# Kernel tuning notes

Hardware: AMD Instinct MI355X
Metric: run time of the kernel (lower is better)

## Reference

```python
import jax, jax.numpy as jnp
import numpy as np
from jax import lax

T, B, D = 200, 1024, 128  # max_len, batch, units (= input feature dim)


def setup_inputs() -> dict:
    key = jax.random.key(0)
    ks = jax.random.split(key, 16)
    s = 1.0 / np.sqrt(D)
    inp = {
        "inputs": jax.random.normal(ks[0], (T, B, D), dtype=jnp.float32),
        "state": jnp.zeros((B, D), dtype=jnp.float32),
        "att_score": jax.random.uniform(ks[1], (T, B, 1), dtype=jnp.float32),
        # binary validity mask [B, T], float because it multiplies the state
        "mask": (jax.random.uniform(ks[2], (B, T)) < 0.9).astype(jnp.float32),
        "max_len": T,
        # u gate (Bilinear: Dense(a) with bias + Dense(b) no bias)
        "Wau": jax.random.normal(ks[3], (D, D), dtype=jnp.float32) * s,
        "bau": jnp.zeros((D,), dtype=jnp.float32),
        "Wbu": jax.random.normal(ks[4], (D, D), dtype=jnp.float32) * s,
        # r gate
        "War": jax.random.normal(ks[5], (D, D), dtype=jnp.float32) * s,
        "bar": jnp.zeros((D,), dtype=jnp.float32),
        "Wbr": jax.random.normal(ks[6], (D, D), dtype=jnp.float32) * s,
        # candidate memory
        "Wac": jax.random.normal(ks[7], (D, D), dtype=jnp.float32) * s,
        "bac": jnp.zeros((D,), dtype=jnp.float32),
        "Wbc": jax.random.normal(ks[8], (D, D), dtype=jnp.float32) * s,
    }
    return inp


def reference(inputs, state, att_score, mask, max_len,
              Wau, bau, Wbu, War, bar, Wbr, Wac, bac, Wbc):
    # time-major mask [T, B, 1]
    mask_t = jnp.swapaxes(mask, 0, 1)[:, :, None]

    def step(s, xs):
        x, a, m = xs  # x:[B,D], a:[B,1], m:[B,1]
        u = jax.nn.sigmoid(x @ Wau + bau + s @ Wbu)
        r = jax.nn.sigmoid(x @ War + bar + s @ Wbr)
        c = jnp.tanh(x @ Wac + bac + r * (s @ Wbc))
        u_ = a * u
        new = (1.0 - u_) * s + u_ * c
        s = new * m + s * (1.0 - m)
        return s, None

    final_state, _ = lax.scan(step, state, (inputs, att_score, mask_t))
    return final_state
```

## Files before the change

### kernel.cpp

```cpp
#include <hip/hip_runtime.h>
#include <stdint.h>

#define T_LEN 200
#define B_SZ  1024
#define D_DIM 128
#define LOG2E 1.44269504088896340736f

typedef __bf16 bf16_t;
typedef __bf16 bf16x8 __attribute__((ext_vector_type(8)));
typedef float  f32x4  __attribute__((ext_vector_type(4)));

union BF8 { bf16x8 v; bf16_t e[8]; };

__device__ inline float rcp_f(float x) { return __builtin_amdgcn_rcpf(x); }

__device__ inline uint32_t cvt_pk_bf16(float a, float b) {
  uint32_t r;
  asm("v_cvt_pk_bf16_f32 %0, %1, %2" : "=v"(r) : "v"(a), "v"(b));
  return r;
}

#define BAR_LDS() asm volatile("s_waitcnt lgkmcnt(0)\n\ts_barrier" ::: "memory")

__global__ __launch_bounds__(512, 2) void augru_fused(
    const float* __restrict__ x,
    const float* __restrict__ state,
    const float* __restrict__ att,
    const float* __restrict__ mask,
    const float* __restrict__ Wau, const float* __restrict__ bau,
    const float* __restrict__ Wbu,
    const float* __restrict__ War, const float* __restrict__ bar,
    const float* __restrict__ Wbr,
    const float* __restrict__ Wac, const float* __restrict__ bac,
    const float* __restrict__ Wbc,
    float* __restrict__ out)
{
  __shared__ bf16_t xb[2][2048];
  __shared__ bf16_t sb[2][2048];
  __shared__ float  am_lds[(T_LEN + 1) * 16];

  const int tid = threadIdx.x;
  const int w  = tid >> 6;
  const int l  = tid & 63;
  const int lm = l & 15;
  const int lg = l >> 4;
  const int bb = blockIdx.x;
  const int R0 = bb * 16;
  const int col = w * 16 + lm;

  BF8 xu[4], xr[4], xc[4];
  BF8 su[4], sr[4], sc[4];
#pragma unroll
  for (int kk = 0; kk < 4; ++kk) {
#pragma unroll
    for (int j = 0; j < 8; ++j) {
      int k = kk * 32 + lg * 8 + j;
      xu[kk].e[j] = (bf16_t)(Wau[k * 128 + col] * LOG2E);
      xr[kk].e[j] = (bf16_t)(War[k * 128 + col] * LOG2E);
      xc[kk].e[j] = (bf16_t)(Wac[k * 128 + col] * (2.0f * LOG2E));
      su[kk].e[j] = (bf16_t)(Wbu[k * 128 + col] * LOG2E);
      sr[kk].e[j] = (bf16_t)(Wbr[k * 128 + col] * LOG2E);
      sc[kk].e[j] = (bf16_t)(Wbc[k * 128 + col] * (2.0f * LOG2E));
    }
  }
  const float b_u = bau[col] * LOG2E;
  const float b_r = bar[col] * LOG2E;
  const float b_c = bac[col] * (2.0f * LOG2E);

  const f32x4 biasU = {b_u, b_u, b_u, b_u};
  const f32x4 biasR = {b_r, b_r, b_r, b_r};
  const f32x4 biasC = {b_c, b_c, b_c, b_c};
  const f32x4 zero4 = {0.f, 0.f, 0.f, 0.f};

  for (int idx = tid; idx < (T_LEN + 1) * 16; idx += 512) {
    int t = idx >> 4; if (t > T_LEN - 1) t = T_LEN - 1;
    int row = idx & 15;
    am_lds[idx] = rcp_f(att[t * B_SZ + R0 + row] * mask[(R0 + row) * T_LEN + t]);
  }

  float sreg[4];
#pragma unroll
  for (int i = 0; i < 4; ++i)
    sreg[i] = state[(R0 + lg * 4 + i) * 128 + col];

  for (int idx = tid; idx < 2048; idx += 512) {
    int row = idx >> 7, k = idx & 127;
    sb[0][(k >> 3) * 128 + (row ^ (2 * ((k >> 3) & 1))) * 8 + (k & 7)] =
        (bf16_t)state[(R0 + row) * 128 + k];
  }

  const int srow = tid & 15;
  const int sc4  = tid >> 4;
  const int stg_pos = (sc4 >> 1) * 128 + srow * 8 + (sc4 & 1) * 4;
  const float* xrow = x + (size_t)(R0 + srow) * 128 + sc4 * 4;
  const size_t xstep = (size_t)B_SZ * 128;
  const size_t xoff_max = (size_t)(T_LEN - 1) * xstep;

  {
    float4 v0 = *(const float4*)(xrow);
    float4 v1 = *(const float4*)(xrow + xstep);
    uint2 p0, p1;
    p0.x = cvt_pk_bf16(v0.x, v0.y); p0.y = cvt_pk_bf16(v0.z, v0.w);
    p1.x = cvt_pk_bf16(v1.x, v1.y); p1.y = cvt_pk_bf16(v1.z, v1.w);
    *(uint2*)&xb[0][stg_pos] = p0;
    *(uint2*)&xb[1][stg_pos] = p1;
  }
  float4 xqA = *(const float4*)(xrow + 2 * xstep);
  float4 xqB = *(const float4*)(xrow + 3 * xstep);
  size_t offA = 4 * xstep;
  size_t offB = 5 * xstep;

  __syncthreads();

  f32x4 gU, gR, gC;
  {
    bf16x8 ax[4];
#pragma unroll
    for (int kk = 0; kk < 4; ++kk)
      ax[kk] = *(const bf16x8*)&xb[0][kk * 512 + 8 * l];
    gU = __builtin_amdgcn_mfma_f32_16x16x32_bf16(ax[0], xu[0].v, biasU, 0, 0, 0);
    gR = __builtin_amdgcn_mfma_f32_16x16x32_bf16(ax[0], xr[0].v, biasR, 0, 0, 0);
    gC = __builtin_amdgcn_mfma_f32_16x16x32_bf16(ax[0], xc[0].v, biasC, 0, 0, 0);
#pragma unroll
    for (int kk = 1; kk < 4; ++kk) {
      gU = __builtin_amdgcn_mfma_f32_16x16x32_bf16(ax[kk], xu[kk].v, gU, 0, 0, 0);
      gR = __builtin_amdgcn_mfma_f32_16x16x32_bf16(ax[kk], xr[kk].v, gR, 0, 0, 0);
      gC = __builtin_amdgcn_mfma_f32_16x16x32_bf16(ax[kk], xc[kk].v, gC, 0, 0, 0);
    }
  }
  union F4 { float4 v; float e[4]; } amv, amn;
  amv.v = *(const float4*)&am_lds[lg * 4];
  const float* am_ptr = &am_lds[16 + lg * 4];

  const int lx8   = 8 * (l ^ (2 * (lg & 1)));
  const int psi   = 2 * ((col >> 3) & 1);
  const int wbase = (col >> 3) * 128 + lg * 32 + (col & 7);

  BAR_LDS();

  auto step = [&](int t, float4& xq, size_t& xoff) {
    const int rp = t & 1;

    bf16x8 as_[4];
#pragma unroll
    for (int kk = 0; kk < 4; ++kk)
      as_[kk] = *(const bf16x8*)&sb[rp][kk * 512 + lx8];

    f32x4 aR = __builtin_amdgcn_mfma_f32_16x16x32_bf16(as_[0], sr[0].v, gR, 0, 0, 0);
    f32x4 bC = __builtin_amdgcn_mfma_f32_16x16x32_bf16(as_[0], sc[0].v, zero4, 0, 0, 0);
    f32x4 aU = __builtin_amdgcn_mfma_f32_16x16x32_bf16(as_[0], su[0].v, gU, 0, 0, 0);
#pragma unroll
    for (int kk = 1; kk < 4; ++kk) {
      aR = __builtin_amdgcn_mfma_f32_16x16x32_bf16(as_[kk], sr[kk].v, aR, 0, 0, 0);
      bC = __builtin_amdgcn_mfma_f32_16x16x32_bf16(as_[kk], sc[kk].v, bC, 0, 0, 0);
      aU = __builtin_amdgcn_mfma_f32_16x16x32_bf16(as_[kk], su[kk].v, aU, 0, 0, 0);
    }

    bf16_t* wbuf = sb[rp ^ 1];
#pragma unroll
    for (int i = 0; i < 4; ++i) {
      float Xr = __builtin_amdgcn_exp2f(-aR[i]);
      float Xu = __builtin_amdgcn_exp2f(-aU[i]);
      float r  = rcp_f(1.0f + Xr);
      float k  = rcp_f(fmaf(Xu, amv.e[i], amv.e[i]));
      float wc = fmaf(r, bC[i], gC[i]);
      float cg = fmaf(-2.0f, rcp_f(__builtin_amdgcn_exp2f(wc) + 1.0f), 1.0f);
      float sf = fmaf(k, cg - sreg[i], sreg[i]);
      sreg[i] = sf;
      wbuf[wbase + 8 * (i ^ psi)] = (bf16_t)sf;
    }

    bf16x8 ax[4];
#pragma unroll
    for (int kk = 0; kk < 4; ++kk)
      ax[kk] = *(const bf16x8*)&xb[rp ^ 1][kk * 512 + 8 * l];

    f32x4 nU = __builtin_amdgcn_mfma_f32_16x16x32_bf16(ax[0], xu[0].v, biasU, 0, 0, 0);
    f32x4 nR = __builtin_amdgcn_mfma_f32_16x16x32_bf16(ax[0], xr[0].v, biasR, 0, 0, 0);
    f32x4 nC = __builtin_amdgcn_mfma_f32_16x16x32_bf16(ax[0], xc[0].v, biasC, 0, 0, 0);
#pragma unroll
    for (int kk = 1; kk < 4; ++kk) {
      nU = __builtin_amdgcn_mfma_f32_16x16x32_bf16(ax[kk], xu[kk].v, nU, 0, 0, 0);
      nR = __builtin_amdgcn_mfma_f32_16x16x32_bf16(ax[kk], xr[kk].v, nR, 0, 0, 0);
      nC = __builtin_amdgcn_mfma_f32_16x16x32_bf16(ax[kk], xc[kk].v, nC, 0, 0, 0);
    }

    {
      uint2 p;
      p.x = cvt_pk_bf16(xq.x, xq.y);
      p.y = cvt_pk_bf16(xq.z, xq.w);
      *(uint2*)&xb[rp][stg_pos] = p;
    }
    xq = *(const float4*)(xrow + xoff);
    xoff += 2 * xstep; if (xoff > xoff_max) xoff = xoff_max;

    amn.v = *(const float4*)am_ptr;
    am_ptr += 16;

    gU = nU; gR = nR; gC = nC;
    amv.v = amn.v;

    BAR_LDS();
  };

#pragma unroll 1
  for (int t = 0; t < T_LEN; t += 2) {
    step(t,     xqA, offA);
    step(t + 1, xqB, offB);
  }

#pragma unroll
  for (int i = 0; i < 4; ++i)
    out[(R0 + lg * 4 + i) * 128 + col] = sreg[i];
}

extern "C" void kernel_launch(void* const* d_in, const int* in_sizes, int n_in,
                              void* d_out, int out_size, void* d_ws, size_t ws_size,
                              hipStream_t stream)
{
  const float* x    = (const float*)d_in[0];
  const float* st   = (const float*)d_in[1];
  const float* att  = (const float*)d_in[2];
  const float* mask = (const float*)d_in[3];
  const float* Wau  = (const float*)d_in[5];
  const float* bau  = (const float*)d_in[6];
  const float* Wbu  = (const float*)d_in[7];
  const float* War  = (const float*)d_in[8];
  const float* bar  = (const float*)d_in[9];
  const float* Wbr  = (const float*)d_in[10];
  const float* Wac  = (const float*)d_in[11];
  const float* bac  = (const float*)d_in[12];
  const float* Wbc  = (const float*)d_in[13];

  (void)d_ws; (void)ws_size;

  augru_fused<<<dim3(64), dim3(512), 0, stream>>>(
      x, st, att, mask, Wau, bau, Wbu, War, bar, Wbr, Wac, bac, Wbc,
      (float*)d_out);
}
```

Baseline: 294.1 us.

## Load x fragments directly into MFMA registers, dropping LDS staging of inputs

The input sequence x is now read from global memory straight into each lane's MFMA operand layout (8 floats per lane per k-chunk) and converted to bf16 in registers, one step ahead. This removes the xb LDS double-buffer along with its stores and reads. The next-step input MFMAs are also moved ahead of the elementwise gate math so they overlap the recurrent MFMAs. The trade-off is more registers for in-flight prefetches (32 floats per lane) and less coalesced global loads, which may hurt occupancy or latency hiding.

```diff
diff --git a/kernel.cpp b/kernel.cpp
--- a/kernel.cpp
+++ b/kernel.cpp
@@ -35,7 +35,6 @@
     const float* __restrict__ Wbc,
     float* __restrict__ out)
 {
-  __shared__ bf16_t xb[2][2048];
   __shared__ bf16_t sb[2][2048];
   __shared__ float  am_lds[(T_LEN + 1) * 16];
 
@@ -89,35 +88,41 @@
         (bf16_t)state[(R0 + row) * 128 + k];
   }
 
-  const int srow = tid & 15;
-  const int sc4  = tid >> 4;
-  const int stg_pos = (sc4 >> 1) * 128 + srow * 8 + (sc4 & 1) * 4;
-  const float* xrow = x + (size_t)(R0 + srow) * 128 + sc4 * 4;
+  struct XF { float4 a[4]; float4 b[4]; };
+  const float* xf = x + (size_t)(R0 + lm) * 128 + lg * 8;
   const size_t xstep = (size_t)B_SZ * 128;
   const size_t xoff_max = (size_t)(T_LEN - 1) * xstep;
 
-  {
-    float4 v0 = *(const float4*)(xrow);
-    float4 v1 = *(const float4*)(xrow + xstep);
-    uint2 p0, p1;
-    p0.x = cvt_pk_bf16(v0.x, v0.y); p0.y = cvt_pk_bf16(v0.z, v0.w);
-    p1.x = cvt_pk_bf16(v1.x, v1.y); p1.y = cvt_pk_bf16(v1.z, v1.w);
-    *(uint2*)&xb[0][stg_pos] = p0;
-    *(uint2*)&xb[1][stg_pos] = p1;
-  }
-  float4 xqA = *(const float4*)(xrow + 2 * xstep);
-  float4 xqB = *(const float4*)(xrow + 3 * xstep);
-  size_t offA = 4 * xstep;
-  size_t offB = 5 * xstep;
+  auto load_frags = [&](XF& f, size_t off) {
+#pragma unroll
+    for (int kk = 0; kk < 4; ++kk) {
+      f.a[kk] = *(const float4*)(xf + off + kk * 32);
+      f.b[kk] = *(const float4*)(xf + off + kk * 32 + 4);
+    }
+  };
+  auto cvt_frags = [&](const XF& f, bf16x8* ax) {
+#pragma unroll
+    for (int kk = 0; kk < 4; ++kk) {
+      union { uint32_t u[4]; bf16x8 v; } p;
+      p.u[0] = cvt_pk_bf16(f.a[kk].x, f.a[kk].y);
+      p.u[1] = cvt_pk_bf16(f.a[kk].z, f.a[kk].w);
+      p.u[2] = cvt_pk_bf16(f.b[kk].x, f.b[kk].y);
+      p.u[3] = cvt_pk_bf16(f.b[kk].z, f.b[kk].w);
+      ax[kk] = p.v;
+    }
+  };
+
+  XF f0, fA;
+  load_frags(f0, 0);
+  load_frags(fA, xstep);
+  size_t offF = 2 * xstep;
 
   __syncthreads();
 
   f32x4 gU, gR, gC;
   {
     bf16x8 ax[4];
-#pragma unroll
-    for (int kk = 0; kk < 4; ++kk)
-      ax[kk] = *(const bf16x8*)&xb[0][kk * 512 + 8 * l];
+    cvt_frags(f0, ax);
     gU = __builtin_amdgcn_mfma_f32_16x16x32_bf16(ax[0], xu[0].v, biasU, 0, 0, 0);
     gR = __builtin_amdgcn_mfma_f32_16x16x32_bf16(ax[0], xr[0].v, biasR, 0, 0, 0);
     gC = __builtin_amdgcn_mfma_f32_16x16x32_bf16(ax[0], xc[0].v, biasC, 0, 0, 0);
@@ -136,15 +141,21 @@
   const int psi   = 2 * ((col >> 3) & 1);
   const int wbase = (col >> 3) * 128 + lg * 32 + (col & 7);
 
-  BAR_LDS();
-
-  auto step = [&](int t, float4& xq, size_t& xoff) {
+  auto step = [&](int t) {
     const int rp = t & 1;
+
+    bf16x8 ax[4];
+    cvt_frags(fA, ax);
+    load_frags(fA, offF);
+    offF += xstep; if (offF > xoff_max) offF = xoff_max;
 
     bf16x8 as_[4];
 #pragma unroll
     for (int kk = 0; kk < 4; ++kk)
       as_[kk] = *(const bf16x8*)&sb[rp][kk * 512 + lx8];
+
+    amn.v = *(const float4*)am_ptr;
+    am_ptr += 16;
 
     f32x4 aR = __builtin_amdgcn_mfma_f32_16x16x32_bf16(as_[0], sr[0].v, gR, 0, 0, 0);
     f32x4 bC = __builtin_amdgcn_mfma_f32_16x16x32_bf16(as_[0], sc[0].v, zero4, 0, 0, 0);
@@ -154,6 +165,16 @@
       aR = __builtin_amdgcn_mfma_f32_16x16x32_bf16(as_[kk], sr[kk].v, aR, 0, 0, 0);
       bC = __builtin_amdgcn_mfma_f32_16x16x32_bf16(as_[kk], sc[kk].v, bC, 0, 0, 0);
       aU = __builtin_amdgcn_mfma_f32_16x16x32_bf16(as_[kk], su[kk].v, aU, 0, 0, 0);
+    }
+
+    f32x4 nU = __builtin_amdgcn_mfma_f32_16x16x32_bf16(ax[0], xu[0].v, biasU, 0, 0, 0);
+    f32x4 nR = __builtin_amdgcn_mfma_f32_16x16x32_bf16(ax[0], xr[0].v, biasR, 0, 0, 0);
+    f32x4 nC = __builtin_amdgcn_mfma_f32_16x16x32_bf16(ax[0], xc[0].v, biasC, 0, 0, 0);
+#pragma unroll
+    for (int kk = 1; kk < 4; ++kk) {
+      nU = __builtin_amdgcn_mfma_f32_16x16x32_bf16(ax[kk], xu[kk].v, nU, 0, 0, 0);
+      nR = __builtin_amdgcn_mfma_f32_16x16x32_bf16(ax[kk], xr[kk].v, nR, 0, 0, 0);
+      nC = __builtin_amdgcn_mfma_f32_16x16x32_bf16(ax[kk], xc[kk].v, nC, 0, 0, 0);
     }
 
     bf16_t* wbuf = sb[rp ^ 1];
@@ -170,33 +191,6 @@
       wbuf[wbase + 8 * (i ^ psi)] = (bf16_t)sf;
     }
 
-    bf16x8 ax[4];
-#pragma unroll
-    for (int kk = 0; kk < 4; ++kk)
-      ax[kk] = *(const bf16x8*)&xb[rp ^ 1][kk * 512 + 8 * l];
-
-    f32x4 nU = __builtin_amdgcn_mfma_f32_16x16x32_bf16(ax[0], xu[0].v, biasU, 0, 0, 0);
-    f32x4 nR = __builtin_amdgcn_mfma_f32_16x16x32_bf16(ax[0], xr[0].v, biasR, 0, 0, 0);
-    f32x4 nC = __builtin_amdgcn_mfma_f32_16x16x32_bf16(ax[0], xc[0].v, biasC, 0, 0, 0);
-#pragma unroll
-    for (int kk = 1; kk < 4; ++kk) {
-      nU = __builtin_amdgcn_mfma_f32_16x16x32_bf16(ax[kk], xu[kk].v, nU, 0, 0, 0);
-      nR = __builtin_amdgcn_mfma_f32_16x16x32_bf16(ax[kk], xr[kk].v, nR, 0, 0, 0);
-      nC = __builtin_amdgcn_mfma_f32_16x16x32_bf16(ax[kk], xc[kk].v, nC, 0, 0, 0);
-    }
-
-    {
-      uint2 p;
-      p.x = cvt_pk_bf16(xq.x, xq.y);
-      p.y = cvt_pk_bf16(xq.z, xq.w);
-      *(uint2*)&xb[rp][stg_pos] = p;
-    }
-    xq = *(const float4*)(xrow + xoff);
-    xoff += 2 * xstep; if (xoff > xoff_max) xoff = xoff_max;
-
-    amn.v = *(const float4*)am_ptr;
-    am_ptr += 16;
-
     gU = nU; gR = nR; gC = nC;
     amv.v = amn.v;
 
@@ -205,8 +199,8 @@
 
 #pragma unroll 1
   for (int t = 0; t < T_LEN; t += 2) {
-    step(t,     xqA, offA);
-    step(t + 1, xqB, offB);
+    step(t);
+    step(t + 1);
   }
 
 #pragma unroll
```

New measurement: 563.6 us. +91.6%, slower.
